# Performance work log

Measured on AMD Instinct MI355X. Metric: run time of the kernel, lower is better.

Reference implementation:

```python
import jax, jax.numpy as jnp
import numpy as np

B, T, C, U, W = 8, 2048, 512, 512, 2


def setup_inputs() -> dict:
    key = jax.random.key(0)
    k1, k2 = jax.random.split(key)
    x = jax.random.normal(k1, (B, T, C), dtype=jnp.float32)
    # Conv1D kernel: [window, in_channels, 3*units] (z, f, o gates), glorot-ish scale
    kernel = jax.random.normal(k2, (W, C, 3 * U), dtype=jnp.float32) * (1.0 / np.sqrt(W * C))
    bias = jnp.zeros((3 * U,), dtype=jnp.float32)
    initial_state = jnp.zeros((1, U), dtype=jnp.float32)
    return {"x": x, "kernel": kernel, "bias": bias, "initial_state": initial_state}


def reference(x, kernel, bias, initial_state):
    # Causal Conv1D: pad (window-1) on the left of the time axis.
    window = kernel.shape[0]
    gates = jax.lax.conv_general_dilated(
        x, kernel,
        window_strides=(1,),
        padding=[(window - 1, 0)],
        dimension_numbers=("NWC", "WIO", "NWC"),
    ) + bias  # [B, T, 3U]
    z, f, o = jnp.split(gates, 3, axis=-1)
    z = jnp.tanh(z)
    f = jax.nn.sigmoid(f)
    o = jax.nn.sigmoid(o)

    # fo-pool recurrence: h_t = f_t * h_{t-1} + (1 - f_t) * z_t
    h0 = jnp.repeat(initial_state, x.shape[0], axis=0)  # [B, U]
    fs = jnp.moveaxis(f, 1, 0)  # [T, B, U]
    zs = jnp.moveaxis(z, 1, 0)  # [T, B, U]

    def step(h, fz):
        f_t, z_t = fz
        h = f_t * h + (1.0 - f_t) * z_t
        return h, h

    _, hs = jax.lax.scan(step, h0, (fs, zs))  # hs: [T, B, U]
    recurrent = jnp.moveaxis(hs, 0, 1)  # [B, T, U]

    # output gate, return_sequences=True
    return recurrent * o
```

## Files before the change

kernel.cpp:

```cpp
#include <hip/hip_runtime.h>


#define Bn 8
#define Tn 2048
#define Cn 512
#define Un 512
#define Nn 1536
#define Kn 1024
#define Mn (Bn * Tn)
#define NC 32
#define CL 64

using bf16x8 = __attribute__((ext_vector_type(8))) __bf16;
using f32x4  = __attribute__((ext_vector_type(4))) float;

__device__ __forceinline__ void async16(const void* g, void* l) {
  __builtin_amdgcn_global_load_lds((const __attribute__((address_space(1))) void*)g,
                                   (__attribute__((address_space(3))) void*)l, 16, 0, 0);
}

__device__ __forceinline__ unsigned short f2bf(float v) {
  union { float f; unsigned u; } c; c.f = v;
  unsigned u = c.u;
  return (unsigned short)((u + 0x7fffu + ((u >> 16) & 1u)) >> 16);
}

__device__ __forceinline__ float fast_sigmoid(float x) {
  float e = __builtin_amdgcn_exp2f(-1.4426950408889634f * x);
  return __builtin_amdgcn_rcpf(1.0f + e);
}
__device__ __forceinline__ float fast_tanh(float x) {
  float e = __builtin_amdgcn_exp2f(-2.8853900817779268f * x);
  return 2.0f * __builtin_amdgcn_rcpf(1.0f + e) - 1.0f;
}

__global__ __launch_bounds__(256) void conv_x(const float* __restrict__ x,
                                              unsigned short* __restrict__ xb) {
  int idx = blockIdx.x * 256 + threadIdx.x;
  int c4  = idx & 127;
  int row = idx >> 7;
  int b   = row / (Tn + 1);
  int t   = row - b * (Tn + 1);
  ushort4 ov;
  if (t == 0) {
    ov.x = ov.y = ov.z = ov.w = 0;
  } else {
    float4 v = *(const float4*)(x + (size_t)(b * Tn + t - 1) * Cn + c4 * 4);
    ov.x = f2bf(v.x); ov.y = f2bf(v.y); ov.z = f2bf(v.z); ov.w = f2bf(v.w);
  }
  *(ushort4*)(xb + (size_t)row * Cn + c4 * 4) = ov;
}

__global__ __launch_bounds__(256) void conv_k(const float* __restrict__ kern,
                                              unsigned short* __restrict__ kT) {
  __shared__ float tile[32][33];
  int kb = blockIdx.x, nb = blockIdx.y;
  int tx = threadIdx.x & 31, ty = threadIdx.x >> 5;
#pragma unroll
  for (int i = 0; i < 4; i++)
    tile[ty + i * 8][tx] = kern[(size_t)(kb * 32 + ty + i * 8) * Nn + nb * 32 + tx];
  __syncthreads();
#pragma unroll
  for (int i = 0; i < 4; i++) {
    int n = nb * 32 + ty + i * 8;
    int k = kb * 32 + tx;
    kT[(size_t)n * Kn + k] = f2bf(tile[tx][ty + i * 8]);
  }
}

__global__ __launch_bounds__(256) void gemm_gates(const unsigned short* __restrict__ xb,
                                                  const unsigned short* __restrict__ kT,
                                                  const float* __restrict__ bias,
                                                  float* __restrict__ gates) {
  __shared__ unsigned short As[128 * 32];
  __shared__ unsigned short Bs[128 * 32];
  const int tid = threadIdx.x;
  const int m0 = blockIdx.x * 128;
  const int n0 = blockIdx.y * 128;
  const int batch = m0 / Tn;
  const int lane = tid & 63;
  const int w = tid >> 6, wr = w >> 1, wc = w & 1;

  const unsigned short* aSrc = xb + (size_t)(m0 + batch + (tid >> 2)) * Cn + (tid & 3) * 8;
  const unsigned short* bSrc = kT + (size_t)(n0 + (tid >> 2)) * Kn + (tid & 3) * 8;

  f32x4 zero = {0.f, 0.f, 0.f, 0.f};
  f32x4 acc[4][4];
#pragma unroll
  for (int i = 0; i < 4; i++)
#pragma unroll
    for (int j = 0; j < 4; j++) acc[i][j] = zero;

  for (int k0 = 0; k0 < Kn; k0 += 32) {
    async16(aSrc + k0,            &As[tid * 8]);
    async16(aSrc + 64 * Cn + k0,  &As[2048 + tid * 8]);
    async16(bSrc + k0,            &Bs[tid * 8]);
    async16(bSrc + 64 * Kn + k0,  &Bs[2048 + tid * 8]);
    __builtin_amdgcn_s_waitcnt(0);
    __syncthreads();

    const int kq = (lane >> 4) * 8;
    const int rA = wr * 64 + (lane & 15);
    const int rB = wc * 64 + (lane & 15);
    bf16x8 af[4], bf[4];
#pragma unroll
    for (int i = 0; i < 4; i++) af[i] = *(const bf16x8*)&As[(rA + i * 16) * 32 + kq];
#pragma unroll
    for (int j = 0; j < 4; j++) bf[j] = *(const bf16x8*)&Bs[(rB + j * 16) * 32 + kq];
#pragma unroll
    for (int i = 0; i < 4; i++)
#pragma unroll
      for (int j = 0; j < 4; j++)
        acc[i][j] = __builtin_amdgcn_mfma_f32_16x16x32_bf16(af[i], bf[j], acc[i][j], 0, 0, 0);
    __syncthreads();
  }

  const int region = blockIdx.y >> 2;
  const int rowB = wr * 64 + (lane >> 4) * 4;
  const int colB = wc * 64 + (lane & 15);
#pragma unroll
  for (int i = 0; i < 4; i++)
#pragma unroll
    for (int j = 0; j < 4; j++)
#pragma unroll
      for (int r = 0; r < 4; r++) {
        int mm = m0 + rowB + i * 16 + r;
        int nn = n0 + colB + j * 16;
        float g = acc[i][j][r] + bias[nn];
        float a = (region == 0) ? fast_tanh(g) : fast_sigmoid(g);
        gates[(size_t)mm * Nn + nn] = a;
      }
}

__global__ __launch_bounds__(512) void scan_phaseA(const float* __restrict__ gates,
                                                   float* __restrict__ aArr,
                                                   float* __restrict__ bArr) {
  int u = threadIdx.x;
  int blk = blockIdx.x;
  int b = blk >> 5, c = blk & (NC - 1);
  const float* gp = gates + (size_t)(b * Tn + c * CL) * Nn;
  float a = 1.0f, bv = 0.0f;
#pragma unroll 4
  for (int t = 0; t < CL; t++) {
    float z = gp[u];
    float f = gp[Un + u];
    a *= f;
    bv = f * bv + (1.0f - f) * z;
    gp += Nn;
  }
  aArr[(size_t)blk * Un + u] = a;
  bArr[(size_t)blk * Un + u] = bv;
}

__global__ __launch_bounds__(256) void scan_phaseB(const float* __restrict__ aArr,
                                                   const float* __restrict__ bArr,
                                                   const float* __restrict__ init,
                                                   float* __restrict__ hstart) {
  int idx = blockIdx.x * 256 + threadIdx.x;
  int b = idx >> 9, u = idx & (Un - 1);
  float h = init[u];
  for (int c = 0; c < NC; c++) {
    size_t offc = (size_t)(b * NC + c) * Un + u;
    hstart[offc] = h;
    h = aArr[offc] * h + bArr[offc];
  }
}

__global__ __launch_bounds__(512) void scan_phaseC(const float* __restrict__ gates,
                                                   const float* __restrict__ hstart,
                                                   float* __restrict__ out) {
  int u = threadIdx.x;
  int blk = blockIdx.x;
  int b = blk >> 5, c = blk & (NC - 1);
  const float* gp = gates + (size_t)(b * Tn + c * CL) * Nn;
  float* op = out + (size_t)(b * Tn + c * CL) * Un;
  float h = hstart[(size_t)blk * Un + u];
#pragma unroll 4
  for (int t = 0; t < CL; t++) {
    float z = gp[u];
    float f = gp[Un + u];
    float o = gp[2 * Un + u];
    h = f * h + (1.0f - f) * z;
    op[u] = h * o;
    gp += Nn;
    op += Un;
  }
}

extern "C" void kernel_launch(void* const* d_in, const int* in_sizes, int n_in,
                              void* d_out, int out_size, void* d_ws, size_t ws_size,
                              hipStream_t stream) {
  const float* x    = (const float*)d_in[0];
  const float* kern = (const float*)d_in[1];
  const float* bias = (const float*)d_in[2];
  const float* init = (const float*)d_in[3];
  float* out = (float*)d_out;

  char* ws = (char*)d_ws;
  unsigned short* xb = (unsigned short*)ws;
  size_t off = (size_t)Bn * (Tn + 1) * Cn * 2;
  unsigned short* kT = (unsigned short*)(ws + off);
  off += (size_t)Nn * Kn * 2;
  float* gates = (float*)(ws + off);
  off += (size_t)Mn * Nn * 4;
  float* aArr = (float*)(ws + off);  off += (size_t)Bn * NC * Un * 4;
  float* bArr = (float*)(ws + off);  off += (size_t)Bn * NC * Un * 4;
  float* hstart = (float*)(ws + off);

  conv_x<<<(Bn * (Tn + 1) * Cn / 4) / 256, 256, 0, stream>>>(x, xb);
  conv_k<<<dim3(32, 48), 256, 0, stream>>>(kern, kT);
  gemm_gates<<<dim3(Mn / 128, Nn / 128), 256, 0, stream>>>(xb, kT, bias, gates);
  scan_phaseA<<<Bn * NC, 512, 0, stream>>>(gates, aArr, bArr);
  scan_phaseB<<<(Bn * Un) / 256, 256, 0, stream>>>(aArr, bArr, init, hstart);
  scan_phaseC<<<Bn * NC, 512, 0, stream>>>(gates, hstart, out);
}
```

Measured before the change: 188.1 us.

## Widen GEMM K-tile to 64 with XOR-swizzled LDS, vectorize scan phases

The gate GEMM now stages 64-wide K slices into LDS using an XOR swizzle on the column chunk. This halves the number of barrier-synchronised iterations and is meant to avoid LDS bank conflicts on the fragment reads. The scan phases A and C now process four units per thread with float4 loads and stores, using 128-thread blocks. The scan is also split into 64 chunks of 32 steps to expose more blocks. The doubled LDS footprint may reduce occupancy, and the extra chunks lengthen the serial phase B loop.

```diff
diff --git a/kernel.cpp b/kernel.cpp
--- a/kernel.cpp
+++ b/kernel.cpp
@@ -8,8 +8,8 @@
 #define Nn 1536
 #define Kn 1024
 #define Mn (Bn * Tn)
-#define NC 32
-#define CL 64
+#define NC 64
+#define CL 32
 
 using bf16x8 = __attribute__((ext_vector_type(8))) __bf16;
 using f32x4  = __attribute__((ext_vector_type(4))) float;
@@ -72,8 +72,8 @@
                                                   const unsigned short* __restrict__ kT,
                                                   const float* __restrict__ bias,
                                                   float* __restrict__ gates) {
-  __shared__ unsigned short As[128 * 32];
-  __shared__ unsigned short Bs[128 * 32];
+  __shared__ unsigned short As[128 * 64];
+  __shared__ unsigned short Bs[128 * 64];
   const int tid = threadIdx.x;
   const int m0 = blockIdx.x * 128;
   const int n0 = blockIdx.y * 128;
@@ -81,8 +81,10 @@
   const int lane = tid & 63;
   const int w = tid >> 6, wr = w >> 1, wc = w & 1;
 
-  const unsigned short* aSrc = xb + (size_t)(m0 + batch + (tid >> 2)) * Cn + (tid & 3) * 8;
-  const unsigned short* bSrc = kT + (size_t)(n0 + (tid >> 2)) * Kn + (tid & 3) * 8;
+  const int srow = (w << 3) + (lane >> 3);
+  const int skq  = (lane & 7) ^ (lane >> 3);
+  const unsigned short* aStage = xb + (size_t)(m0 + batch + srow) * Cn + (skq << 3);
+  const unsigned short* bStage = kT + (size_t)(n0 + srow) * Kn + (skq << 3);
 
   f32x4 zero = {0.f, 0.f, 0.f, 0.f};
   f32x4 acc[4][4];
@@ -91,27 +93,34 @@
 #pragma unroll
     for (int j = 0; j < 4; j++) acc[i][j] = zero;
 
-  for (int k0 = 0; k0 < Kn; k0 += 32) {
-    async16(aSrc + k0,            &As[tid * 8]);
-    async16(aSrc + 64 * Cn + k0,  &As[2048 + tid * 8]);
-    async16(bSrc + k0,            &Bs[tid * 8]);
-    async16(bSrc + 64 * Kn + k0,  &Bs[2048 + tid * 8]);
+  const int rA0 = wr * 64 + (lane & 15);
+  const int rB0 = wc * 64 + (lane & 15);
+  const int swz = lane & 7;
+
+  for (int k0 = 0; k0 < Kn; k0 += 64) {
+#pragma unroll
+    for (int j = 0; j < 4; j++) {
+      async16(aStage + (size_t)(j << 5) * Cn + k0, &As[(j * 256 + tid) * 8]);
+      async16(bStage + (size_t)(j << 5) * Kn + k0, &Bs[(j * 256 + tid) * 8]);
+    }
     __builtin_amdgcn_s_waitcnt(0);
     __syncthreads();
 
-    const int kq = (lane >> 4) * 8;
-    const int rA = wr * 64 + (lane & 15);
-    const int rB = wc * 64 + (lane & 15);
-    bf16x8 af[4], bf[4];
-#pragma unroll
-    for (int i = 0; i < 4; i++) af[i] = *(const bf16x8*)&As[(rA + i * 16) * 32 + kq];
-#pragma unroll
-    for (int j = 0; j < 4; j++) bf[j] = *(const bf16x8*)&Bs[(rB + j * 16) * 32 + kq];
-#pragma unroll
-    for (int i = 0; i < 4; i++)
-#pragma unroll
-      for (int j = 0; j < 4; j++)
-        acc[i][j] = __builtin_amdgcn_mfma_f32_16x16x32_bf16(af[i], bf[j], acc[i][j], 0, 0, 0);
+#pragma unroll
+    for (int ks = 0; ks < 2; ks++) {
+      const int col = (((ks << 2) + (lane >> 4)) ^ swz) << 3;
+      bf16x8 af[4], bf[4];
+#pragma unroll
+      for (int i = 0; i < 4; i++) {
+        af[i] = *(const bf16x8*)&As[(rA0 + i * 16) * 64 + col];
+        bf[i] = *(const bf16x8*)&Bs[(rB0 + i * 16) * 64 + col];
+      }
+#pragma unroll
+      for (int i = 0; i < 4; i++)
+#pragma unroll
+        for (int j = 0; j < 4; j++)
+          acc[i][j] = __builtin_amdgcn_mfma_f32_16x16x32_bf16(af[i], bf[j], acc[i][j], 0, 0, 0);
+    }
     __syncthreads();
   }
 
@@ -132,24 +141,27 @@
       }
 }
 
-__global__ __launch_bounds__(512) void scan_phaseA(const float* __restrict__ gates,
+__global__ __launch_bounds__(128) void scan_phaseA(const float* __restrict__ gates,
                                                    float* __restrict__ aArr,
                                                    float* __restrict__ bArr) {
-  int u = threadIdx.x;
+  int u4 = threadIdx.x * 4;
   int blk = blockIdx.x;
-  int b = blk >> 5, c = blk & (NC - 1);
+  int b = blk >> 6, c = blk & (NC - 1);
   const float* gp = gates + (size_t)(b * Tn + c * CL) * Nn;
-  float a = 1.0f, bv = 0.0f;
+  float4 a = {1.f, 1.f, 1.f, 1.f}, bv = {0.f, 0.f, 0.f, 0.f};
 #pragma unroll 4
   for (int t = 0; t < CL; t++) {
-    float z = gp[u];
-    float f = gp[Un + u];
-    a *= f;
-    bv = f * bv + (1.0f - f) * z;
+    float4 z = *(const float4*)(gp + u4);
+    float4 f = *(const float4*)(gp + Un + u4);
+    a.x *= f.x; a.y *= f.y; a.z *= f.z; a.w *= f.w;
+    bv.x = f.x * bv.x + (1.0f - f.x) * z.x;
+    bv.y = f.y * bv.y + (1.0f - f.y) * z.y;
+    bv.z = f.z * bv.z + (1.0f - f.z) * z.z;
+    bv.w = f.w * bv.w + (1.0f - f.w) * z.w;
     gp += Nn;
   }
-  aArr[(size_t)blk * Un + u] = a;
-  bArr[(size_t)blk * Un + u] = bv;
+  *(float4*)(aArr + (size_t)blk * Un + u4) = a;
+  *(float4*)(bArr + (size_t)blk * Un + u4) = bv;
 }
 
 __global__ __launch_bounds__(256) void scan_phaseB(const float* __restrict__ aArr,
@@ -166,22 +178,27 @@
   }
 }
 
-__global__ __launch_bounds__(512) void scan_phaseC(const float* __restrict__ gates,
+__global__ __launch_bounds__(128) void scan_phaseC(const float* __restrict__ gates,
                                                    const float* __restrict__ hstart,
                                                    float* __restrict__ out) {
-  int u = threadIdx.x;
+  int u4 = threadIdx.x * 4;
   int blk = blockIdx.x;
-  int b = blk >> 5, c = blk & (NC - 1);
+  int b = blk >> 6, c = blk & (NC - 1);
   const float* gp = gates + (size_t)(b * Tn + c * CL) * Nn;
   float* op = out + (size_t)(b * Tn + c * CL) * Un;
-  float h = hstart[(size_t)blk * Un + u];
+  float4 h = *(const float4*)(hstart + (size_t)blk * Un + u4);
 #pragma unroll 4
   for (int t = 0; t < CL; t++) {
-    float z = gp[u];
-    float f = gp[Un + u];
-    float o = gp[2 * Un + u];
-    h = f * h + (1.0f - f) * z;
-    op[u] = h * o;
+    float4 z = *(const float4*)(gp + u4);
+    float4 f = *(const float4*)(gp + Un + u4);
+    float4 o = *(const float4*)(gp + 2 * Un + u4);
+    h.x = f.x * h.x + (1.0f - f.x) * z.x;
+    h.y = f.y * h.y + (1.0f - f.y) * z.y;
+    h.z = f.z * h.z + (1.0f - f.z) * z.z;
+    h.w = f.w * h.w + (1.0f - f.w) * z.w;
+    float4 ov;
+    ov.x = h.x * o.x; ov.y = h.y * o.y; ov.z = h.z * o.z; ov.w = h.w * o.w;
+    *(float4*)(op + u4) = ov;
     gp += Nn;
     op += Un;
   }
@@ -210,7 +227,7 @@
   conv_x<<<(Bn * (Tn + 1) * Cn / 4) / 256, 256, 0, stream>>>(x, xb);
   conv_k<<<dim3(32, 48), 256, 0, stream>>>(kern, kT);
   gemm_gates<<<dim3(Mn / 128, Nn / 128), 256, 0, stream>>>(xb, kT, bias, gates);
-  scan_phaseA<<<Bn * NC, 512, 0, stream>>>(gates, aArr, bArr);
+  scan_phaseA<<<Bn * NC, 128, 0, stream>>>(gates, aArr, bArr);
   scan_phaseB<<<(Bn * Un) / 256, 256, 0, stream>>>(aArr, bArr, init, hstart);
-  scan_phaseC<<<Bn * NC, 512, 0, stream>>>(gates, hstart, out);
-}
+  scan_phaseC<<<Bn * NC, 128, 0, stream>>>(gates, hstart, out);
+}
```

Result: no change. 187.7 us (-0.2%).
